# Optimization experiments

Hardware: AMD Instinct MI355X
Metric: run time of the kernel (lower is better)

## Reference

```python
import jax, jax.numpy as jnp
import numpy as np

B, C, H, W = 4, 512, 64, 64
NUM_GROUPS = 32
EPS = 1e-6


def setup_inputs() -> dict:
    key = jax.random.key(0)
    ks = jax.random.split(key, 5)
    s = 1.0 / np.sqrt(C)
    return {
        "x": jax.random.normal(ks[0], (B, C, H, W), dtype=jnp.float32),
        "gn_scale": jnp.ones((C,), jnp.float32),
        "gn_bias": jnp.zeros((C,), jnp.float32),
        "wq": jax.random.normal(ks[1], (C, C), jnp.float32) * s,
        "bq": jnp.zeros((C,), jnp.float32),
        "wk": jax.random.normal(ks[2], (C, C), jnp.float32) * s,
        "bk": jnp.zeros((C,), jnp.float32),
        "wv": jax.random.normal(ks[3], (C, C), jnp.float32) * s,
        "bv": jnp.zeros((C,), jnp.float32),
        "wo": jax.random.normal(ks[4], (C, C), jnp.float32) * s,
        "bo": jnp.zeros((C,), jnp.float32),
    }


def _group_norm(x, scale, bias):
    # x: [b, c, h, w]; normalize over (c//g, h, w) within each of g groups
    b, c, h, w = x.shape
    g = NUM_GROUPS
    xg = x.reshape(b, g, c // g, h, w)
    mean = jnp.mean(xg, axis=(2, 3, 4), keepdims=True)
    var = jnp.var(xg, axis=(2, 3, 4), keepdims=True)
    xg = (xg - mean) * jax.lax.rsqrt(var + EPS)
    xn = xg.reshape(b, c, h, w)
    return xn * scale[None, :, None, None] + bias[None, :, None, None]


def _conv1x1(x, w, b):
    # channel-mixing 1x1 conv: [b, c, h, w] x [c_in, c_out] -> [b, c_out, h, w]
    return jnp.einsum('bchw,cd->bdhw', x, w) + b[None, :, None, None]


def reference(x, gn_scale, gn_bias, wq, bq, wk, bk, wv, bv, wo, bo):
    b, c, h, w = x.shape
    h_ = _group_norm(x, gn_scale, gn_bias)
    q = _conv1x1(h_, wq, bq).reshape(b, c, h * w).transpose(0, 2, 1)  # [b, hw, c]
    k = _conv1x1(h_, wk, bk).reshape(b, c, h * w)                     # [b, c, hw]
    v = _conv1x1(h_, wv, bv).reshape(b, c, h * w)                     # [b, c, hw]
    scores = jnp.matmul(q, k) * (c ** -0.5)      # [b, hw, hw]
    attn = jax.nn.softmax(scores, axis=-1)       # [b, hw, hw]
    out = jnp.matmul(v, attn.transpose(0, 2, 1)) # [b, c, hw]
    out = out.reshape(b, c, h, w)
    out = _conv1x1(out, wo, bo)
    return x + out
```

## Files before the change

### kernel.cpp

```cpp
#include <hip/hip_runtime.h>
#include <stdint.h>

#define S_ 4096

typedef __attribute__((ext_vector_type(8))) short short8;
typedef __attribute__((ext_vector_type(4))) float f32x4;

__device__ __forceinline__ short cvt_bf16(float f) {
  uint32_t u = __builtin_bit_cast(uint32_t, f);
  u += 0x7FFFu + ((u >> 16) & 1u);
  return (short)(u >> 16);
}

__device__ __forceinline__ void gload_lds16(const void* g, void* l) {
  __builtin_amdgcn_global_load_lds(
      (const __attribute__((address_space(1))) void*)g,
      (__attribute__((address_space(3))) void*)l, 16, 0, 0);
}

__global__ __launch_bounds__(256) void k_transpose_w(const float* __restrict__ src,
                                                     short* __restrict__ dst) {
  __shared__ float t[32][33];
  int n0 = blockIdx.x * 32, c0 = blockIdx.y * 32;
  int lx = threadIdx.x & 31, ly = threadIdx.x >> 5;
#pragma unroll
  for (int i = 0; i < 4; ++i) {
    int c = ly + i * 8;
    t[c][lx] = src[(size_t)(c0 + c) * 512 + n0 + lx];
  }
  __syncthreads();
#pragma unroll
  for (int i = 0; i < 4; ++i) {
    int n = ly + i * 8;
    dst[(size_t)(n0 + n) * 512 + c0 + lx] = cvt_bf16(t[lx][n]);
  }
}

__global__ void k_bias_concat(const float* __restrict__ bq, const float* __restrict__ bk,
                              float* __restrict__ bqk) {
  int i = blockIdx.x * 256 + threadIdx.x;
  if (i < 512) bqk[i] = bq[i];
  else if (i < 1024) bqk[i] = bk[i - 512];
}

__global__ __launch_bounds__(256) void k_gn_stats(const float* __restrict__ x,
                                                  float* __restrict__ stats) {
  int bg = blockIdx.x;
  const float* p = x + (size_t)bg * 65536;
  float s = 0.f, ss = 0.f;
#pragma unroll 4
  for (int i = 0; i < 64; ++i) {
    float4 v = *(const float4*)(p + i * 1024 + threadIdx.x * 4);
    s += v.x + v.y + v.z + v.w;
    ss += v.x * v.x + v.y * v.y + v.z * v.z + v.w * v.w;
  }
#pragma unroll
  for (int m = 1; m < 64; m <<= 1) {
    s += __shfl_xor(s, m, 64);
    ss += __shfl_xor(ss, m, 64);
  }
  __shared__ float red[8];
  int w = threadIdx.x >> 6;
  if ((threadIdx.x & 63) == 0) { red[w * 2] = s; red[w * 2 + 1] = ss; }
  __syncthreads();
  if (threadIdx.x == 0) {
    float S1 = red[0] + red[2] + red[4] + red[6];
    float S2 = red[1] + red[3] + red[5] + red[7];
    float mean = S1 * (1.f / 65536.f);
    float var = S2 * (1.f / 65536.f) - mean * mean;
    stats[bg * 2] = mean;
    stats[bg * 2 + 1] = rsqrtf(var + 1e-6f);
  }
}

__global__ __launch_bounds__(256) void k_gn_apply(const float* __restrict__ x,
    const float* __restrict__ stats, const float* __restrict__ gsc,
    const float* __restrict__ gbi, short* __restrict__ h_t) {
  __shared__ float t[64][65];
  int p0 = blockIdx.x * 64, c0 = blockIdx.y * 64, b = blockIdx.z;
  int lp = threadIdx.x & 63, lc = threadIdx.x >> 6;
#pragma unroll
  for (int i = 0; i < 16; ++i) {
    int c = c0 + lc * 16 + i;
    float mean = stats[(b * 32 + (c >> 4)) * 2];
    float rstd = stats[(b * 32 + (c >> 4)) * 2 + 1];
    float v = x[((size_t)b * 512 + c) * 4096 + p0 + lp];
    t[lc * 16 + i][lp] = (v - mean) * rstd * gsc[c] + gbi[c];
  }
  __syncthreads();
  int pl = threadIdx.x >> 2;
  int cs = (threadIdx.x & 3) * 16;
  short8 v8a, v8b;
#pragma unroll
  for (int j = 0; j < 8; ++j) v8a[j] = cvt_bf16(t[cs + j][pl]);
#pragma unroll
  for (int j = 0; j < 8; ++j) v8b[j] = cvt_bf16(t[cs + 8 + j][pl]);
  size_t o = ((size_t)(b * 4096 + p0 + pl)) * 512 + c0 + cs;
  *(short8*)(h_t + o) = v8a;
  *(short8*)(h_t + o + 8) = v8b;
}

template <int BIAS_M, int FINAL>
__global__ __launch_bounds__(256) void k_gemm(const short* __restrict__ A,
    const short* __restrict__ Bm, const float* __restrict__ bias,
    short* __restrict__ Cb, float* __restrict__ Cf, const float* __restrict__ resid,
    int ldc) {
  __shared__ __align__(16) short a_lds[128 * 32];
  __shared__ __align__(16) short b_lds[128 * 32];
  int m0 = blockIdx.x * 128, n0 = blockIdx.y * 128;
  int lane = threadIdx.x & 63, wid = threadIdx.x >> 6;
  int h16 = lane >> 4, l16 = lane & 15;
  int wr = wid >> 1, wc = wid & 1;
  int srow = lane >> 2, sslot = lane & 3;

  f32x4 acc[4][4];
#pragma unroll
  for (int mi = 0; mi < 4; ++mi)
#pragma unroll
    for (int ni = 0; ni < 4; ++ni) acc[mi][ni] = (f32x4){0.f, 0.f, 0.f, 0.f};

  for (int kk = 0; kk < 16; ++kk) {
#pragma unroll
    for (int i = 0; i < 2; ++i) {
      int r0 = (wid * 2 + i) * 16;
      gload_lds16(A + ((size_t)(m0 + r0 + srow)) * 512 + kk * 32 + sslot * 8, a_lds + r0 * 32);
      gload_lds16(Bm + ((size_t)(n0 + r0 + srow)) * 512 + kk * 32 + sslot * 8, b_lds + r0 * 32);
    }
    asm volatile("s_waitcnt vmcnt(0)" ::: "memory");
    __syncthreads();
    short8 af[4], bf[4];
#pragma unroll
    for (int mi = 0; mi < 4; ++mi)
      af[mi] = *(const short8*)(a_lds + (wr * 64 + mi * 16 + l16) * 32 + h16 * 8);
#pragma unroll
    for (int ni = 0; ni < 4; ++ni)
      bf[ni] = *(const short8*)(b_lds + (wc * 64 + ni * 16 + l16) * 32 + h16 * 8);
#pragma unroll
    for (int mi = 0; mi < 4; ++mi)
#pragma unroll
      for (int ni = 0; ni < 4; ++ni)
        acc[mi][ni] = __builtin_amdgcn_mfma_f32_16x16x32_bf16(af[mi], bf[ni], acc[mi][ni], 0, 0, 0);
    __syncthreads();
  }

#pragma unroll
  for (int mi = 0; mi < 4; ++mi)
#pragma unroll
    for (int ni = 0; ni < 4; ++ni)
#pragma unroll
      for (int r = 0; r < 4; ++r) {
        int row = m0 + wr * 64 + mi * 16 + 4 * h16 + r;
        int col = n0 + wc * 64 + ni * 16 + l16;
        float v = acc[mi][ni][r] + (BIAS_M ? bias[row] : bias[col]);
        if (FINAL) {
          size_t oidx = ((size_t)((col >> 12) * 512 + row)) * 4096 + (col & 4095);
          Cf[oidx] = v + resid[oidx];
        } else {
          Cb[(size_t)row * ldc + col] = cvt_bf16(v);
        }
      }
}

__global__ __launch_bounds__(512, 2) void k_flash(const short* __restrict__ qk,
    const short* __restrict__ v_t, short* __restrict__ o_attn) {
  __shared__ __align__(16) short k_lds[64 * 520];
  __shared__ __align__(16) short v_lds[512 * 64];
  __shared__ __align__(16) short p_lds[64 * 72];
  __shared__ float red_m[64][2];
  __shared__ float red_l[64][2];

  int b = blockIdx.y, qt = blockIdx.x;
  int lane = threadIdx.x & 63, wid = threadIdx.x >> 6;
  int h16 = lane >> 4, l16 = lane & 15;
  int wr = wid >> 1, wc = wid & 1;
  const float K2 = 1.4426950408889634f / 22.627416997969522f;

  const short* qbase = qk + ((size_t)(b * 4096 + qt * 64 + wr * 16 + l16)) * 1024;
  short8 qf[16];
#pragma unroll
  for (int kk = 0; kk < 16; ++kk) qf[kk] = *(const short8*)(qbase + kk * 32 + h16 * 8);

  float m_run[4], l_run[4];
#pragma unroll
  for (int r = 0; r < 4; ++r) { m_run[r] = -3.0e38f; l_run[r] = 0.f; }
  f32x4 oacc[16];
#pragma unroll
  for (int cf = 0; cf < 16; ++cf) oacc[cf] = (f32x4){0.f, 0.f, 0.f, 0.f};

  int vrow_off = lane >> 3;
  int vslot = (lane & 7) ^ (vrow_off & 7);

  for (int kt = 0; kt < 64; ++kt) {
    int kv0 = kt * 64;
#pragma unroll
    for (int rr = 0; rr < 8; ++rr) {
      int row = wid * 8 + rr;
      gload_lds16(qk + ((size_t)(b * 4096 + kv0 + row)) * 1024 + 512 + lane * 8,
                  k_lds + row * 520);
    }
#pragma unroll
    for (int ii = 0; ii < 8; ++ii) {
      int i = wid * 8 + ii;
      int d = i * 8 + vrow_off;
      gload_lds16(v_t + (size_t)d * 16384 + (b * 4096 + kv0) + vslot * 8, v_lds + i * 512);
    }
    asm volatile("s_waitcnt vmcnt(0)" ::: "memory");
    __syncthreads();

    f32x4 sc[2];
    sc[0] = (f32x4){0.f, 0.f, 0.f, 0.f};
    sc[1] = (f32x4){0.f, 0.f, 0.f, 0.f};
#pragma unroll
    for (int kk = 0; kk < 16; ++kk) {
#pragma unroll
      for (int c = 0; c < 2; ++c) {
        short8 kf = *(const short8*)(k_lds + (wc * 32 + c * 16 + l16) * 520 + kk * 32 + h16 * 8);
        sc[c] = __builtin_amdgcn_mfma_f32_16x16x32_bf16(qf[kk], kf, sc[c], 0, 0, 0);
      }
    }
    float mt[4];
#pragma unroll
    for (int r = 0; r < 4; ++r) mt[r] = fmaxf(sc[0][r], sc[1][r]);
#pragma unroll
    for (int m = 1; m < 16; m <<= 1)
#pragma unroll
      for (int r = 0; r < 4; ++r) mt[r] = fmaxf(mt[r], __shfl_xor(mt[r], m, 64));
    if (l16 == 0)
#pragma unroll
      for (int r = 0; r < 4; ++r) red_m[wr * 16 + 4 * h16 + r][wc] = mt[r];
    __syncthreads();

    float mn[4], resc[4], ls[4];
#pragma unroll
    for (int r = 0; r < 4; ++r) {
      int row = wr * 16 + 4 * h16 + r;
      float mfull = fmaxf(red_m[row][0], red_m[row][1]);
      mn[r] = fmaxf(m_run[r], mfull);
      resc[r] = exp2f((m_run[r] - mn[r]) * K2);
      m_run[r] = mn[r];
      ls[r] = 0.f;
    }
#pragma unroll
    for (int c = 0; c < 2; ++c)
#pragma unroll
      for (int r = 0; r < 4; ++r) {
        float p = exp2f((sc[c][r] - mn[r]) * K2);
        ls[r] += p;
        p_lds[(wr * 16 + 4 * h16 + r) * 72 + wc * 32 + c * 16 + l16] = cvt_bf16(p);
      }
#pragma unroll
    for (int m = 1; m < 16; m <<= 1)
#pragma unroll
      for (int r = 0; r < 4; ++r) ls[r] += __shfl_xor(ls[r], m, 64);
    if (l16 == 0)
#pragma unroll
      for (int r = 0; r < 4; ++r) red_l[wr * 16 + 4 * h16 + r][wc] = ls[r];
    __syncthreads();

#pragma unroll
    for (int r = 0; r < 4; ++r) {
      int row = wr * 16 + 4 * h16 + r;
      l_run[r] = l_run[r] * resc[r] + red_l[row][0] + red_l[row][1];
    }
#pragma unroll
    for (int cf = 0; cf < 16; ++cf)
#pragma unroll
      for (int r = 0; r < 4; ++r) oacc[cf][r] *= resc[r];

#pragma unroll
    for (int ks = 0; ks < 2; ++ks) {
      short8 pa = *(const short8*)(p_lds + (wr * 16 + l16) * 72 + ks * 32 + h16 * 8);
#pragma unroll
      for (int cf = 0; cf < 16; ++cf) {
        int dcol = wc * 256 + cf * 16 + l16;
        short8 vb = *(const short8*)(v_lds + dcol * 64 + (((ks * 4 + h16) ^ (l16 & 7)) * 8));
        oacc[cf] = __builtin_amdgcn_mfma_f32_16x16x32_bf16(pa, vb, oacc[cf], 0, 0, 0);
      }
    }
    __syncthreads();
  }

  float inv[4];
#pragma unroll
  for (int r = 0; r < 4; ++r) inv[r] = 1.f / l_run[r];
#pragma unroll
  for (int cf = 0; cf < 16; ++cf)
#pragma unroll
    for (int r = 0; r < 4; ++r) {
      int row = b * 4096 + qt * 64 + wr * 16 + 4 * h16 + r;
      int col = wc * 256 + cf * 16 + l16;
      o_attn[(size_t)row * 512 + col] = cvt_bf16(oacc[cf][r] * inv[r]);
    }
}

extern "C" void kernel_launch(void* const* d_in, const int* in_sizes, int n_in,
                              void* d_out, int out_size, void* d_ws, size_t ws_size,
                              hipStream_t stream) {
  const float* x   = (const float*)d_in[0];
  const float* gsc = (const float*)d_in[1];
  const float* gbi = (const float*)d_in[2];
  const float* wq  = (const float*)d_in[3];
  const float* bq  = (const float*)d_in[4];
  const float* wk  = (const float*)d_in[5];
  const float* bk  = (const float*)d_in[6];
  const float* wv  = (const float*)d_in[7];
  const float* bv  = (const float*)d_in[8];
  const float* wo  = (const float*)d_in[9];
  const float* bo  = (const float*)d_in[10];
  float* out = (float*)d_out;

  char* ws = (char*)d_ws;
  float* stats = (float*)ws;
  float* bqk   = (float*)(ws + 4096);
  short* wqk_t = (short*)(ws + 16384);
  short* wv_t  = (short*)(ws + 16384 + (1u << 20));
  short* wo_t  = (short*)(ws + 16384 + (1u << 20) + (1u << 19));
  char*  big   = ws + 16384 + (1u << 21);
  short* h_t   = (short*)big;
  short* qkb   = (short*)(big + (16ll << 20));
  short* v_t   = (short*)(big + (48ll << 20));
  short* o_at  = (short*)(big + (64ll << 20));

  dim3 b256(256);
  k_transpose_w<<<dim3(16, 16), b256, 0, stream>>>(wq, wqk_t);
  k_transpose_w<<<dim3(16, 16), b256, 0, stream>>>(wk, wqk_t + 512 * 512);
  k_transpose_w<<<dim3(16, 16), b256, 0, stream>>>(wv, wv_t);
  k_transpose_w<<<dim3(16, 16), b256, 0, stream>>>(wo, wo_t);
  k_bias_concat<<<4, 256, 0, stream>>>(bq, bk, bqk);
  k_gn_stats<<<128, b256, 0, stream>>>(x, stats);
  k_gn_apply<<<dim3(64, 8, 4), b256, 0, stream>>>(x, stats, gsc, gbi, h_t);
  k_gemm<0, 0><<<dim3(128, 8), b256, 0, stream>>>(h_t, wqk_t, bqk, qkb, nullptr, nullptr, 1024);
  k_gemm<1, 0><<<dim3(4, 128), b256, 0, stream>>>(wv_t, h_t, bv, v_t, nullptr, nullptr, 16384);
  k_flash<<<dim3(64, 4), dim3(512), 0, stream>>>(qkb, v_t, o_at);
  k_gemm<1, 1><<<dim3(4, 128), b256, 0, stream>>>(wo_t, o_at, bo, nullptr, out, x, 0);
}
```

Measured before the change: 395.0 us.

## Split-KV flash attention with 32x32 MFMA, lazy rescaling and combine pass

Replaces the flash attention kernel with a split-KV version. Each query tile of 128 rows processes half of the keys, and a new combine kernel merges the two partial outputs using the stored running max and sum. Inside the kernel it switches to 32x32x16 MFMA with a head-dim split across wave pairs, reduces partial scores through LDS, and skips the accumulator rescale unless the row max grows by more than a threshold. It also prefetches the next K tile and the next double-width V tile while computing. The aim is to fill the GPU with more blocks and cut MFMA and softmax overhead, at the cost of an extra kernel, extra partial-output traffic, and reusing the h_t buffer as scratch.

```diff
diff --git a/kernel.cpp b/kernel.cpp
--- a/kernel.cpp
+++ b/kernel.cpp
@@ -1,15 +1,19 @@
 #include <hip/hip_runtime.h>
 #include <stdint.h>
 
-#define S_ 4096
-
 typedef __attribute__((ext_vector_type(8))) short short8;
 typedef __attribute__((ext_vector_type(4))) float f32x4;
+typedef __attribute__((ext_vector_type(16))) float f32x16;
+typedef __attribute__((ext_vector_type(2))) unsigned int uint2v;
 
 __device__ __forceinline__ short cvt_bf16(float f) {
   uint32_t u = __builtin_bit_cast(uint32_t, f);
   u += 0x7FFFu + ((u >> 16) & 1u);
   return (short)(u >> 16);
+}
+
+__device__ __forceinline__ float bf16_to_f32(short s) {
+  return __builtin_bit_cast(float, (uint32_t)((unsigned short)s) << 16);
 }
 
 __device__ __forceinline__ void gload_lds16(const void* g, void* l) {
@@ -161,136 +165,190 @@
       }
 }
 
-__global__ __launch_bounds__(512, 2) void k_flash(const short* __restrict__ qk,
-    const short* __restrict__ v_t, short* __restrict__ o_attn) {
-  __shared__ __align__(16) short k_lds[64 * 520];
+__global__ __launch_bounds__(512, 2) void k_flash2(const short* __restrict__ qk,
+    const short* __restrict__ v_t, short* __restrict__ oa, short* __restrict__ ob,
+    float* __restrict__ ml) {
+  __shared__ __align__(16) short k_lds[32 * 512];
   __shared__ __align__(16) short v_lds[512 * 64];
-  __shared__ __align__(16) short p_lds[64 * 72];
-  __shared__ float red_m[64][2];
-  __shared__ float red_l[64][2];
-
-  int b = blockIdx.y, qt = blockIdx.x;
-  int lane = threadIdx.x & 63, wid = threadIdx.x >> 6;
-  int h16 = lane >> 4, l16 = lane & 15;
-  int wr = wid >> 1, wc = wid & 1;
-  const float K2 = 1.4426950408889634f / 22.627416997969522f;
-
-  const short* qbase = qk + ((size_t)(b * 4096 + qt * 64 + wr * 16 + l16)) * 1024;
+  __shared__ __align__(16) float s_lds[8 * 1024];
+  __shared__ __align__(16) short p_lds[128 * 40];
+
+  const int tid = threadIdx.x;
+  const int lane = tid & 63, wid = tid >> 6;
+  const int qg = wid >> 1, dh = wid & 1;
+  const int l31 = lane & 31, h = lane >> 5;
+  const int bx = blockIdx.x;
+  const int combo = bx & 7, qt = bx >> 3;
+  const int b = combo >> 1, s = combo & 1;
+  const float K2 = 0.06376649f;
+
   short8 qf[16];
-#pragma unroll
-  for (int kk = 0; kk < 16; ++kk) qf[kk] = *(const short8*)(qbase + kk * 32 + h16 * 8);
-
-  float m_run[4], l_run[4];
-#pragma unroll
-  for (int r = 0; r < 4; ++r) { m_run[r] = -3.0e38f; l_run[r] = 0.f; }
-  f32x4 oacc[16];
-#pragma unroll
-  for (int cf = 0; cf < 16; ++cf) oacc[cf] = (f32x4){0.f, 0.f, 0.f, 0.f};
-
-  int vrow_off = lane >> 3;
-  int vslot = (lane & 7) ^ (vrow_off & 7);
-
-  for (int kt = 0; kt < 64; ++kt) {
-    int kv0 = kt * 64;
-#pragma unroll
-    for (int rr = 0; rr < 8; ++rr) {
-      int row = wid * 8 + rr;
-      gload_lds16(qk + ((size_t)(b * 4096 + kv0 + row)) * 1024 + 512 + lane * 8,
-                  k_lds + row * 520);
-    }
-#pragma unroll
-    for (int ii = 0; ii < 8; ++ii) {
-      int i = wid * 8 + ii;
-      int d = i * 8 + vrow_off;
-      gload_lds16(v_t + (size_t)d * 16384 + (b * 4096 + kv0) + vslot * 8, v_lds + i * 512);
-    }
-    asm volatile("s_waitcnt vmcnt(0)" ::: "memory");
-    __syncthreads();
-
-    f32x4 sc[2];
-    sc[0] = (f32x4){0.f, 0.f, 0.f, 0.f};
-    sc[1] = (f32x4){0.f, 0.f, 0.f, 0.f};
-#pragma unroll
-    for (int kk = 0; kk < 16; ++kk) {
-#pragma unroll
-      for (int c = 0; c < 2; ++c) {
-        short8 kf = *(const short8*)(k_lds + (wc * 32 + c * 16 + l16) * 520 + kk * 32 + h16 * 8);
-        sc[c] = __builtin_amdgcn_mfma_f32_16x16x32_bf16(qf[kk], kf, sc[c], 0, 0, 0);
-      }
-    }
-    float mt[4];
-#pragma unroll
-    for (int r = 0; r < 4; ++r) mt[r] = fmaxf(sc[0][r], sc[1][r]);
-#pragma unroll
-    for (int m = 1; m < 16; m <<= 1)
-#pragma unroll
-      for (int r = 0; r < 4; ++r) mt[r] = fmaxf(mt[r], __shfl_xor(mt[r], m, 64));
-    if (l16 == 0)
-#pragma unroll
-      for (int r = 0; r < 4; ++r) red_m[wr * 16 + 4 * h16 + r][wc] = mt[r];
-    __syncthreads();
-
-    float mn[4], resc[4], ls[4];
-#pragma unroll
-    for (int r = 0; r < 4; ++r) {
-      int row = wr * 16 + 4 * h16 + r;
-      float mfull = fmaxf(red_m[row][0], red_m[row][1]);
-      mn[r] = fmaxf(m_run[r], mfull);
-      resc[r] = exp2f((m_run[r] - mn[r]) * K2);
-      m_run[r] = mn[r];
-      ls[r] = 0.f;
-    }
-#pragma unroll
-    for (int c = 0; c < 2; ++c)
-#pragma unroll
-      for (int r = 0; r < 4; ++r) {
-        float p = exp2f((sc[c][r] - mn[r]) * K2);
-        ls[r] += p;
-        p_lds[(wr * 16 + 4 * h16 + r) * 72 + wc * 32 + c * 16 + l16] = cvt_bf16(p);
-      }
-#pragma unroll
-    for (int m = 1; m < 16; m <<= 1)
-#pragma unroll
-      for (int r = 0; r < 4; ++r) ls[r] += __shfl_xor(ls[r], m, 64);
-    if (l16 == 0)
-#pragma unroll
-      for (int r = 0; r < 4; ++r) red_l[wr * 16 + 4 * h16 + r][wc] = ls[r];
-    __syncthreads();
-
-#pragma unroll
-    for (int r = 0; r < 4; ++r) {
-      int row = wr * 16 + 4 * h16 + r;
-      l_run[r] = l_run[r] * resc[r] + red_l[row][0] + red_l[row][1];
-    }
-#pragma unroll
-    for (int cf = 0; cf < 16; ++cf)
-#pragma unroll
-      for (int r = 0; r < 4; ++r) oacc[cf][r] *= resc[r];
-
+  {
+    const short* qbase = qk + ((size_t)(b * 4096 + qt * 128 + qg * 32 + l31)) * 1024
+                         + dh * 256 + h * 8;
+#pragma unroll
+    for (int ks = 0; ks < 16; ++ks) qf[ks] = *(const short8*)(qbase + ks * 16);
+  }
+  asm volatile("s_waitcnt vmcnt(0)" ::: "memory");
+
+  const size_t kvrow0 = (size_t)(b * 4096 + s * 2048);
+
+#define STAGE_K(T)                                                                    \
+  {                                                                                   \
+    int t_ = (T);                                                                     \
+    _Pragma("unroll") for (int i = 0; i < 4; ++i) {                                   \
+      int row = wid * 4 + i;                                                          \
+      gload_lds16(qk + (kvrow0 + t_ * 32 + row) * 1024 + 512 + ((lane ^ (row & 7)) * 8), \
+                  k_lds + row * 512);                                                 \
+    }                                                                                 \
+  }
+#define STAGE_V(P)                                                                    \
+  {                                                                                   \
+    int p_ = (P);                                                                     \
+    _Pragma("unroll") for (int ii = 0; ii < 8; ++ii) {                                \
+      int d = wid * 64 + ii * 8 + (lane >> 3);                                        \
+      gload_lds16(v_t + (size_t)d * 16384 + (b * 4096 + s * 2048 + p_ * 64)           \
+                      + (((lane & 7) ^ (d & 7)) * 8),                                 \
+                  v_lds + (wid * 8 + ii) * 512);                                      \
+    }                                                                                 \
+  }
+
+  STAGE_K(0);
+  STAGE_V(0);
+  asm volatile("s_waitcnt vmcnt(8)" ::: "memory");
+  __builtin_amdgcn_s_barrier();
+  __builtin_amdgcn_sched_barrier(0);
+
+  float m_run = -3.0e38f, l_run = 0.f;
+  f32x16 acc[8];
+#pragma unroll
+  for (int tl = 0; tl < 8; ++tl)
+#pragma unroll
+    for (int r = 0; r < 16; ++r) acc[tl][r] = 0.f;
+
+  for (int t = 0; t < 64; ++t) {
+    f32x16 st;
+#pragma unroll
+    for (int r = 0; r < 16; ++r) st[r] = 0.f;
+#pragma unroll
+    for (int ks = 0; ks < 16; ++ks) {
+      int c = dh * 32 + ks * 2 + h;
+      short8 kf = *(const short8*)(k_lds + l31 * 512 + ((c ^ (l31 & 7)) * 8));
+      st = __builtin_amdgcn_mfma_f32_32x32x16_bf16(kf, qf[ks], st, 0, 0, 0);
+    }
+    {
+      float* sp = s_lds + wid * 1024 + lane * 4;
+#pragma unroll
+      for (int q4 = 0; q4 < 4; ++q4) {
+        f32x4 v = {st[q4 * 4 + 0], st[q4 * 4 + 1], st[q4 * 4 + 2], st[q4 * 4 + 3]};
+        *(f32x4*)(sp + q4 * 256) = v;
+      }
+    }
+    asm volatile("s_waitcnt lgkmcnt(0)" ::: "memory");
+    __builtin_amdgcn_s_barrier();
+    __builtin_amdgcn_sched_barrier(0);
+    STAGE_K(t + 1 < 64 ? t + 1 : 63);
+    {
+      const float* sp = s_lds + (wid ^ 1) * 1024 + lane * 4;
+#pragma unroll
+      for (int q4 = 0; q4 < 4; ++q4) {
+        f32x4 v = *(const f32x4*)(sp + q4 * 256);
+        st[q4 * 4 + 0] += v[0]; st[q4 * 4 + 1] += v[1];
+        st[q4 * 4 + 2] += v[2]; st[q4 * 4 + 3] += v[3];
+      }
+    }
+    float mt = st[0];
+#pragma unroll
+    for (int r = 1; r < 16; ++r) mt = fmaxf(mt, st[r]);
+    mt = fmaxf(mt, __shfl_xor(mt, 32));
+    if (__any(mt > m_run + 45.0f)) {
+      float mnew = fmaxf(m_run, mt);
+      float rs = exp2f((m_run - mnew) * K2);
+      m_run = mnew;
+      l_run *= rs;
+#pragma unroll
+      for (int r = 0; r < 16; ++r) {
+        int rowq = (r & 3) + 8 * (r >> 2) + 4 * h;
+        float rr = __shfl(rs, rowq);
+#pragma unroll
+        for (int tl = 0; tl < 8; ++tl) acc[tl][r] *= rr;
+      }
+    }
+    float ls = 0.f;
+#pragma unroll
+    for (int r = 0; r < 16; ++r) { st[r] = exp2f((st[r] - m_run) * K2); ls += st[r]; }
+    ls += __shfl_xor(ls, 32);
+    l_run += ls;
+    if (dh == 0) {
+      int q = qg * 32 + l31;
+#pragma unroll
+      for (int g = 0; g < 4; ++g) {
+        unsigned int p0, p1;
+        asm("v_cvt_pk_bf16_f32 %0, %1, %2" : "=v"(p0) : "v"(st[4 * g + 0]), "v"(st[4 * g + 1]));
+        asm("v_cvt_pk_bf16_f32 %0, %1, %2" : "=v"(p1) : "v"(st[4 * g + 2]), "v"(st[4 * g + 3]));
+        uint2v w; w[0] = p0; w[1] = p1;
+        *(uint2v*)(p_lds + q * 40 + g * 8 + h * 4) = w;
+      }
+    }
+    asm volatile("s_waitcnt vmcnt(4) lgkmcnt(0)" ::: "memory");
+    __builtin_amdgcn_s_barrier();
+    __builtin_amdgcn_sched_barrier(0);
 #pragma unroll
     for (int ks = 0; ks < 2; ++ks) {
-      short8 pa = *(const short8*)(p_lds + (wr * 16 + l16) * 72 + ks * 32 + h16 * 8);
-#pragma unroll
-      for (int cf = 0; cf < 16; ++cf) {
-        int dcol = wc * 256 + cf * 16 + l16;
-        short8 vb = *(const short8*)(v_lds + dcol * 64 + (((ks * 4 + h16) ^ (l16 & 7)) * 8));
-        oacc[cf] = __builtin_amdgcn_mfma_f32_16x16x32_bf16(pa, vb, oacc[cf], 0, 0, 0);
-      }
-    }
-    __syncthreads();
-  }
-
-  float inv[4];
-#pragma unroll
-  for (int r = 0; r < 4; ++r) inv[r] = 1.f / l_run[r];
-#pragma unroll
-  for (int cf = 0; cf < 16; ++cf)
-#pragma unroll
-    for (int r = 0; r < 4; ++r) {
-      int row = b * 4096 + qt * 64 + wr * 16 + 4 * h16 + r;
-      int col = wc * 256 + cf * 16 + l16;
-      o_attn[(size_t)row * 512 + col] = cvt_bf16(oacc[cf][r] * inv[r]);
-    }
+      short8 pa = *(const short8*)(p_lds + (qg * 32 + l31) * 40 + ks * 16 + h * 8);
+#pragma unroll
+      for (int tl = 0; tl < 8; ++tl) {
+        int d = dh * 256 + tl * 32 + l31;
+        int c = (t & 1) * 4 + ks * 2 + h;
+        short8 vb = *(const short8*)(v_lds + d * 64 + ((c ^ (d & 7)) * 8));
+        acc[tl] = __builtin_amdgcn_mfma_f32_32x32x16_bf16(pa, vb, acc[tl], 0, 0, 0);
+      }
+    }
+    asm volatile("s_waitcnt vmcnt(0) lgkmcnt(0)" ::: "memory");
+    __builtin_amdgcn_s_barrier();
+    __builtin_amdgcn_sched_barrier(0);
+    if (t & 1) STAGE_V(((t + 1) >> 1) < 32 ? ((t + 1) >> 1) : 31);
+  }
+
+  float linv = 1.0f / l_run;
+  short* obuf = (s == 0) ? oa : ob;
+#pragma unroll
+  for (int r = 0; r < 16; ++r) {
+    int rowq = (r & 3) + 8 * (r >> 2) + 4 * h;
+    float li = __shfl(linv, rowq);
+    size_t grow = ((size_t)(b * 4096 + qt * 128 + qg * 32 + rowq)) * 512;
+#pragma unroll
+    for (int tl = 0; tl < 8; ++tl)
+      obuf[grow + dh * 256 + tl * 32 + l31] = cvt_bf16(acc[tl][r] * li);
+  }
+  if (dh == 0 && lane < 32) {
+    int gq = b * 4096 + qt * 128 + qg * 32 + lane;
+    ml[((size_t)s * 16384 + gq) * 2 + 0] = m_run;
+    ml[((size_t)s * 16384 + gq) * 2 + 1] = l_run;
+  }
+#undef STAGE_K
+#undef STAGE_V
+}
+
+__global__ __launch_bounds__(256) void k_combine(const short* __restrict__ oa,
+    const float* __restrict__ ml, short* __restrict__ ob_out) {
+  int gq = blockIdx.x * 4 + (threadIdx.x >> 6);
+  int d0 = (threadIdx.x & 63) * 8;
+  const float K2 = 0.06376649f;
+  float ma = ml[(size_t)gq * 2 + 0], la = ml[(size_t)gq * 2 + 1];
+  float mb = ml[((size_t)16384 + gq) * 2 + 0], lb = ml[((size_t)16384 + gq) * 2 + 1];
+  float m = fmaxf(ma, mb);
+  float ca = exp2f((ma - m) * K2) * la;
+  float cb = exp2f((mb - m) * K2) * lb;
+  float inv = 1.f / (ca + cb);
+  ca *= inv; cb *= inv;
+  short8 a = *(const short8*)(oa + (size_t)gq * 512 + d0);
+  short8 bv = *(const short8*)(ob_out + (size_t)gq * 512 + d0);
+  short8 o;
+#pragma unroll
+  for (int j = 0; j < 8; ++j)
+    o[j] = cvt_bf16(ca * bf16_to_f32(a[j]) + cb * bf16_to_f32(bv[j]));
+  *(short8*)(ob_out + (size_t)gq * 512 + d0) = o;
 }
 
 extern "C" void kernel_launch(void* const* d_in, const int* in_sizes, int n_in,
@@ -320,6 +378,7 @@
   short* qkb   = (short*)(big + (16ll << 20));
   short* v_t   = (short*)(big + (48ll << 20));
   short* o_at  = (short*)(big + (64ll << 20));
+  float* mlbuf = (float*)(big + (80ll << 20));
 
   dim3 b256(256);
   k_transpose_w<<<dim3(16, 16), b256, 0, stream>>>(wq, wqk_t);
@@ -331,6 +390,7 @@
   k_gn_apply<<<dim3(64, 8, 4), b256, 0, stream>>>(x, stats, gsc, gbi, h_t);
   k_gemm<0, 0><<<dim3(128, 8), b256, 0, stream>>>(h_t, wqk_t, bqk, qkb, nullptr, nullptr, 1024);
   k_gemm<1, 0><<<dim3(4, 128), b256, 0, stream>>>(wv_t, h_t, bv, v_t, nullptr, nullptr, 16384);
-  k_flash<<<dim3(64, 4), dim3(512), 0, stream>>>(qkb, v_t, o_at);
+  k_flash2<<<dim3(256), dim3(512), 0, stream>>>(qkb, v_t, h_t, o_at, mlbuf);
+  k_combine<<<dim3(4096), b256, 0, stream>>>(h_t, mlbuf, o_at);
   k_gemm<1, 1><<<dim3(4, 128), b256, 0, stream>>>(wo_t, o_at, bo, nullptr, out, x, 0);
 }
```

New measurement: 369.5 us. 1.07x faster.
